# Kernel tuning notes

Measured on AMD Instinct MI355X. Metric: run time of the kernel, lower is better.

## Reference

```python
import jax, jax.numpy as jnp
import numpy as np

N_NODES = 100000
N_EDGES = 3200000
IN_DIM, HID_DIM, OUT_DIM = 512, 256, 64


def setup_inputs() -> dict:
    key = jax.random.key(0)
    k1, k2, k3, k4, k5, k6 = jax.random.split(key, 6)
    x = jax.random.normal(k1, (N_NODES, IN_DIM), dtype=jnp.float32)
    src = jax.random.randint(k2, (N_EDGES,), 0, N_NODES, dtype=jnp.int32)
    dst = jax.random.randint(k3, (N_EDGES,), 0, N_NODES, dtype=jnp.int32)
    edge_index = jnp.stack([src, dst])  # [2, E]: row 0 = src (column), row 1 = dst (row)
    edge_weight = jax.random.uniform(k4, (N_EDGES,), dtype=jnp.float32)
    # Xavier-uniform init like nn.init.xavier_uniform_
    lim1 = float(np.sqrt(6.0 / (IN_DIM + HID_DIM)))
    lim2 = float(np.sqrt(6.0 / (HID_DIM + OUT_DIM)))
    W1 = jax.random.uniform(k5, (IN_DIM, HID_DIM), minval=-lim1, maxval=lim1, dtype=jnp.float32)
    W2 = jax.random.uniform(k6, (HID_DIM, OUT_DIM), minval=-lim2, maxval=lim2, dtype=jnp.float32)
    return {"x": x, "edge_index": edge_index, "edge_weight": edge_weight, "W1": W1, "W2": W2}


def _spmm(edge_index, edge_weight, support):
    # out[dst] += w * support[src]  (sparse adjacency @ dense support)
    src, dst = edge_index[0], edge_index[1]
    msgs = support[src] * edge_weight[:, None]  # [E, F]
    return jax.ops.segment_sum(msgs, dst, num_segments=N_NODES)


def reference(x, edge_index, edge_weight, W1, W2):
    # Layer 1: dense GEMM then SpMM, then ReLU (dropout is identity in eval)
    h = _spmm(edge_index, edge_weight, x @ W1)
    h = jax.nn.relu(h)
    # Layer 2
    out = _spmm(edge_index, edge_weight, h @ W2)
    return jax.nn.softmax(out, axis=1)
```

## Files before the change

### kernel.cpp

```cpp
#include <hip/hip_runtime.h>
#include <hip/hip_bf16.h>

typedef __attribute__((ext_vector_type(8))) short bf16x8;
typedef __attribute__((ext_vector_type(4))) float f32x4;
typedef __attribute__((ext_vector_type(4))) _Float16 f16x4;
typedef unsigned short ushort_t;

#define NN   100000
#define NE   3200000
#define IND  512
#define HIDD 256
#define OUTD 64

#define NBKT 98
#define P1E  2048

__device__ __forceinline__ ushort_t f2bf(float a) {
    unsigned u = __float_as_uint(a);
    unsigned r = (u + 0x7FFFu + ((u >> 16) & 1u)) >> 16;
    return (ushort_t)r;
}
__device__ __forceinline__ float bf2f(ushort_t b) {
    return __uint_as_float(((unsigned)b) << 16);
}

union U8 { ushort_t us[8]; unsigned u32[4]; uint4 v; };
union U4 { ushort_t us[4]; uint2 v; };

#define GLOAD_LDS16(gp, lp) \
    __builtin_amdgcn_global_load_lds( \
        (const __attribute__((address_space(1))) void*)(const void*)(gp), \
        (__attribute__((address_space(3))) void*)(void*)(lp), 16, 0, 0)

__global__ void splitw_k(const float* __restrict__ in, ushort_t* __restrict__ thi,
                         ushort_t* __restrict__ tlo, int R, int C) {
    int i = blockIdx.x * 256 + threadIdx.x;
    if (i < R * C) {
        int r = i / C, c = i % C;
        float a = in[i];
        ushort_t h = f2bf(a);
        thi[(size_t)c * R + r] = h;
        tlo[(size_t)c * R + r] = f2bf(a - bf2f(h));
    }
}

__global__ __launch_bounds__(256, 3) void gemm1_k(
    const float* __restrict__ A, const ushort_t* __restrict__ BtHi,
    const ushort_t* __restrict__ BtLo, _Float16* __restrict__ C)
{
    const int M = NN, N = HIDD, K = IND;
    __shared__ __align__(16) float    sA [128 * 32];
    __shared__ __align__(16) ushort_t sBh[128 * 32];
    __shared__ __align__(16) ushort_t sBl[128 * 32];

    const int tid  = threadIdx.x;
    const int wave = tid >> 6;
    const int lane = tid & 63;
    const int quad = lane >> 4;
    const int l15  = lane & 15;
    const int wr   = wave >> 1;
    const int wc   = wave & 1;
    const int n0   = blockIdx.x * 128;
    const int m0   = blockIdx.y * 128;

    const float* aSrc[4];
    float*       aDst[4];
    #pragma unroll
    for (int it = 0; it < 4; ++it) {
        int f = it * 256 + tid;
        int r = f >> 3;
        int bp = (f & 7) ^ ((r & 3) << 1) ^ ((r >> 2) & 1);
        int gr = m0 + r; if (gr >= M) gr = M - 1;
        aSrc[it] = A + (size_t)gr * K + bp * 4;
        aDst[it] = &sA[f * 4];
    }
    const ushort_t* bhSrc[2]; const ushort_t* blSrc[2];
    ushort_t* bhDst[2]; ushort_t* blDst[2];
    #pragma unroll
    for (int it = 0; it < 2; ++it) {
        int f = it * 256 + tid;
        int r = f >> 2;
        int qp = (f & 3) ^ ((r >> 1) & 3);
        bhSrc[it] = BtHi + (size_t)(n0 + r) * K + qp * 8;
        blSrc[it] = BtLo + (size_t)(n0 + r) * K + qp * 8;
        bhDst[it] = &sBh[f * 8];
        blDst[it] = &sBl[f * 8];
    }

    int aOff[4][2];
    #pragma unroll
    for (int ms = 0; ms < 4; ++ms) {
        int rA = wr * 64 + ms * 16 + l15;
        int sw = ((rA & 3) << 1) ^ ((rA >> 2) & 1);
        int cb = quad << 1;
        aOff[ms][0] = rA * 32 + (((cb    ) ^ sw) << 2);
        aOff[ms][1] = rA * 32 + (((cb | 1) ^ sw) << 2);
    }
    int bOff[4];
    #pragma unroll
    for (int ns = 0; ns < 4; ++ns) {
        int rB = wc * 64 + ns * 16 + l15;
        bOff[ns] = rB * 32 + (quad ^ ((rB >> 1) & 3)) * 8;
    }

    f32x4 acc[4][4] = {};

    for (int k0 = 0; k0 < K; k0 += 32) {
        #pragma unroll
        for (int it = 0; it < 4; ++it) GLOAD_LDS16(aSrc[it] + k0, aDst[it]);
        #pragma unroll
        for (int it = 0; it < 2; ++it) {
            GLOAD_LDS16(bhSrc[it] + k0, bhDst[it]);
            GLOAD_LDS16(blSrc[it] + k0, blDst[it]);
        }
        __syncthreads();

        bf16x8 aH[4], aL[4];
        #pragma unroll
        for (int ms = 0; ms < 4; ++ms) {
            float4 v0 = *(const float4*)&sA[aOff[ms][0]];
            float4 v1 = *(const float4*)&sA[aOff[ms][1]];
            float vv[8] = {v0.x, v0.y, v0.z, v0.w, v1.x, v1.y, v1.z, v1.w};
            U8 H, L;
            #pragma unroll
            for (int j = 0; j < 4; ++j) {
                unsigned u0 = __float_as_uint(vv[2 * j]);
                unsigned u1 = __float_as_uint(vv[2 * j + 1]);
                H.u32[j] = __builtin_amdgcn_perm(u1, u0, 0x07060302u);
                float r0 = vv[2 * j]     - __uint_as_float(u0 & 0xFFFF0000u);
                float r1 = vv[2 * j + 1] - __uint_as_float(u1 & 0xFFFF0000u);
                L.u32[j] = __builtin_amdgcn_perm(__float_as_uint(r1),
                                                 __float_as_uint(r0), 0x07060302u);
            }
            aH[ms] = *(const bf16x8*)&H.v;
            aL[ms] = *(const bf16x8*)&L.v;
        }

        #pragma unroll
        for (int ns = 0; ns < 4; ++ns) {
            bf16x8 bH = *(const bf16x8*)&sBh[bOff[ns]];
            bf16x8 bL = *(const bf16x8*)&sBl[bOff[ns]];
            #pragma unroll
            for (int ms = 0; ms < 4; ++ms) {
                acc[ms][ns] = __builtin_amdgcn_mfma_f32_16x16x32_bf16(aH[ms], bH, acc[ms][ns], 0, 0, 0);
                acc[ms][ns] = __builtin_amdgcn_mfma_f32_16x16x32_bf16(aL[ms], bH, acc[ms][ns], 0, 0, 0);
                acc[ms][ns] = __builtin_amdgcn_mfma_f32_16x16x32_bf16(aH[ms], bL, acc[ms][ns], 0, 0, 0);
            }
        }
        __syncthreads();
    }

    #pragma unroll
    for (int ms = 0; ms < 4; ++ms) {
        int row = m0 + wr * 64 + ms * 16 + quad * 4;
        #pragma unroll
        for (int ns = 0; ns < 4; ++ns) {
            int col = n0 + wc * 64 + ns * 16 + l15;
            #pragma unroll
            for (int r = 0; r < 4; ++r)
                if (row + r < M) C[(size_t)(row + r) * N + col] = (_Float16)acc[ms][ns][r];
        }
    }
}

__global__ __launch_bounds__(256) void gemm2_k(
    const ushort_t* __restrict__ AHi, const ushort_t* __restrict__ ALo,
    const ushort_t* __restrict__ BtHi, const ushort_t* __restrict__ BtLo,
    _Float16* __restrict__ C)
{
    const int M = NN, N = OUTD, K = HIDD;
    __shared__ __align__(16) ushort_t sAh[128 * 32];
    __shared__ __align__(16) ushort_t sAl[128 * 32];
    __shared__ __align__(16) ushort_t sBh[64 * 32];
    __shared__ __align__(16) ushort_t sBl[64 * 32];

    const int tid  = threadIdx.x;
    const int wave = tid >> 6;
    const int lane = tid & 63;
    const int quad = lane >> 4;
    const int l15  = lane & 15;
    const int m0   = blockIdx.x * 128;

    const ushort_t* ahSrc[2]; const ushort_t* alSrc[2];
    ushort_t* ahDst[2]; ushort_t* alDst[2];
    #pragma unroll
    for (int it = 0; it < 2; ++it) {
        int f = it * 256 + tid;
        int r = f >> 2;
        int qp = (f & 3) ^ ((r >> 1) & 3);
        int gr = m0 + r; if (gr >= M) gr = M - 1;
        ahSrc[it] = AHi + (size_t)gr * K + qp * 8;
        alSrc[it] = ALo + (size_t)gr * K + qp * 8;
        ahDst[it] = &sAh[f * 8];
        alDst[it] = &sAl[f * 8];
    }
    const ushort_t *bhSrc, *blSrc; ushort_t *bhDst, *blDst;
    {
        int f = tid;
        int r = f >> 2;
        int qp = (f & 3) ^ ((r >> 1) & 3);
        bhSrc = BtHi + (size_t)r * K + qp * 8;
        blSrc = BtLo + (size_t)r * K + qp * 8;
        bhDst = &sBh[f * 8];
        blDst = &sBl[f * 8];
    }

    int aOff[2], bOff[4];
    #pragma unroll
    for (int ms = 0; ms < 2; ++ms) {
        int rA = wave * 32 + ms * 16 + l15;
        aOff[ms] = rA * 32 + (quad ^ ((rA >> 1) & 3)) * 8;
    }
    #pragma unroll
    for (int ns = 0; ns < 4; ++ns) {
        int rB = ns * 16 + l15;
        bOff[ns] = rB * 32 + (quad ^ ((rB >> 1) & 3)) * 8;
    }

    f32x4 acc[2][4] = {};

    for (int k0 = 0; k0 < K; k0 += 32) {
        #pragma unroll
        for (int it = 0; it < 2; ++it) {
            GLOAD_LDS16(ahSrc[it] + k0, ahDst[it]);
            GLOAD_LDS16(alSrc[it] + k0, alDst[it]);
        }
        GLOAD_LDS16(bhSrc + k0, bhDst);
        GLOAD_LDS16(blSrc + k0, blDst);
        __syncthreads();

        bf16x8 aH[2], aL[2];
        #pragma unroll
        for (int ms = 0; ms < 2; ++ms) {
            aH[ms] = *(const bf16x8*)&sAh[aOff[ms]];
            aL[ms] = *(const bf16x8*)&sAl[aOff[ms]];
        }
        #pragma unroll
        for (int ns = 0; ns < 4; ++ns) {
            bf16x8 bH = *(const bf16x8*)&sBh[bOff[ns]];
            bf16x8 bL = *(const bf16x8*)&sBl[bOff[ns]];
            #pragma unroll
            for (int ms = 0; ms < 2; ++ms) {
                acc[ms][ns] = __builtin_amdgcn_mfma_f32_16x16x32_bf16(aH[ms], bH, acc[ms][ns], 0, 0, 0);
                acc[ms][ns] = __builtin_amdgcn_mfma_f32_16x16x32_bf16(aL[ms], bH, acc[ms][ns], 0, 0, 0);
                acc[ms][ns] = __builtin_amdgcn_mfma_f32_16x16x32_bf16(aH[ms], bL, acc[ms][ns], 0, 0, 0);
            }
        }
        __syncthreads();
    }

    #pragma unroll
    for (int ms = 0; ms < 2; ++ms) {
        int row = m0 + wave * 32 + ms * 16 + quad * 4;
        #pragma unroll
        for (int ns = 0; ns < 4; ++ns) {
            int col = ns * 16 + l15;
            #pragma unroll
            for (int r = 0; r < 4; ++r)
                if (row + r < M) C[(size_t)(row + r) * N + col] = (_Float16)acc[ms][ns][r];
        }
    }
}

__global__ __launch_bounds__(256) void bhist_k(const int* __restrict__ dst,
                                               int* __restrict__ bucketHist) {
    __shared__ int h[NBKT];
    int t = threadIdx.x;
    if (t < NBKT) h[t] = 0;
    __syncthreads();
    #pragma unroll
    for (int j = 0; j < 4; ++j) {
        int e = blockIdx.x * 1024 + t + j * 256;
        if (e < NE) atomicAdd(&h[dst[e] >> 10], 1);
    }
    __syncthreads();
    if (t < NBKT && h[t]) atomicAdd(&bucketHist[t], h[t]);
}

__global__ __launch_bounds__(128) void bscan_k(const int* __restrict__ bucketHist,
                                               int* __restrict__ bucketStart,
                                               int* __restrict__ bucketCursor) {
    __shared__ int s[128];
    int t = threadIdx.x;
    int v = (t < NBKT) ? bucketHist[t] : 0;
    s[t] = v;
    for (int off = 1; off < 128; off <<= 1) {
        __syncthreads();
        int a = (t >= off) ? s[t - off] : 0;
        __syncthreads();
        s[t] += a;
    }
    __syncthreads();
    if (t < NBKT) { bucketStart[t] = s[t] - v; bucketCursor[t] = s[t] - v; }
    if (t == NBKT - 1) bucketStart[NBKT] = s[t];
}

__global__ __launch_bounds__(256) void phase1_k(
    const int* __restrict__ src, const int* __restrict__ dst,
    const float* __restrict__ w, int* __restrict__ bucketCursor,
    int2* __restrict__ binned)
{
    __shared__ int2 raw[P1E];
    __shared__ int2 ord[P1E];
    __shared__ ushort_t rbkt[P1E], obkt[P1E];
    __shared__ int hist[128], excl[128], cursor[128], gbase[128], stmp[128];

    int t = threadIdx.x;
    if (t < 128) hist[t] = 0;
    __syncthreads();

    int e0 = blockIdx.x * P1E;
    #pragma unroll
    for (int j = 0; j < P1E / 256; ++j) {
        int li = t + j * 256;
        int e = e0 + li;
        if (e < NE) {
            int d = dst[e];
            int b = d >> 10;
            raw[li] = make_int2(src[e] | ((d & 1023) << 17), __float_as_int(w[e]));
            rbkt[li] = (ushort_t)b;
            atomicAdd(&hist[b], 1);
        } else rbkt[li] = 0xFFFFu;
    }
    __syncthreads();
    int v = (t < 128) ? hist[t] : 0;
    if (t < 128) stmp[t] = v;
    for (int off = 1; off < 128; off <<= 1) {
        __syncthreads();
        int a = (t < 128 && t >= off) ? stmp[t - off] : 0;
        __syncthreads();
        if (t < 128) stmp[t] += a;
    }
    __syncthreads();
    if (t < 128) { excl[t] = stmp[t] - v; cursor[t] = stmp[t] - v; }
    if (t < NBKT) gbase[t] = atomicAdd(&bucketCursor[t], hist[t]);
    __syncthreads();
    #pragma unroll
    for (int j = 0; j < P1E / 256; ++j) {
        int li = t + j * 256;
        ushort_t b = rbkt[li];
        if (b != 0xFFFFu) {
            int p = atomicAdd(&cursor[b], 1);
            ord[p] = raw[li];
            obkt[p] = b;
        }
    }
    __syncthreads();
    int tot = excl[NBKT - 1] + hist[NBKT - 1];
    #pragma unroll
    for (int j = 0; j < P1E / 256; ++j) {
        int li = t + j * 256;
        if (li < tot) {
            int b = obkt[li];
            binned[(size_t)gbase[b] + (li - excl[b])] = ord[li];
        }
    }
}

__global__ __launch_bounds__(256) void phase2_k(
    const int* __restrict__ bucketStart, const int2* __restrict__ binned,
    int* __restrict__ rowptr, int2* __restrict__ esw)
{
    __shared__ int cnt[1024], ex[1024], cur[1024], wsum[256];
    int t = threadIdx.x, blk = blockIdx.x;
    int gb = bucketStart[blk], ge = bucketStart[blk + 1];
    #pragma unroll
    for (int j = 0; j < 4; ++j) cnt[t + j * 256] = 0;
    __syncthreads();
    for (int e = gb + t; e < ge; e += 256)
        atomicAdd(&cnt[(binned[e].x >> 17) & 1023], 1);
    __syncthreads();
    int b4 = t * 4;
    int l0 = cnt[b4], l1 = cnt[b4 + 1], l2 = cnt[b4 + 2], l3 = cnt[b4 + 3];
    int ls = l0 + l1 + l2 + l3;
    wsum[t] = ls;
    for (int off = 1; off < 256; off <<= 1) {
        __syncthreads();
        int a = (t >= off) ? wsum[t - off] : 0;
        __syncthreads();
        wsum[t] += a;
    }
    __syncthreads();
    int be = wsum[t] - ls;
    ex[b4] = be;            cur[b4] = be;
    ex[b4 + 1] = be + l0;     cur[b4 + 1] = be + l0;
    ex[b4 + 2] = be + l0 + l1;  cur[b4 + 2] = be + l0 + l1;
    ex[b4 + 3] = be + l0 + l1 + l2; cur[b4 + 3] = be + l0 + l1 + l2;
    __syncthreads();
    int n0 = blk << 10;
    #pragma unroll
    for (int j = 0; j < 4; ++j) {
        int i = b4 + j;
        if (n0 + i < NN) rowptr[n0 + i] = gb + ex[i];
    }
    if (blk == NBKT - 1 && t == 0) rowptr[NN] = NE;
    for (int e = gb + t; e < ge; e += 256) {
        int2 en = binned[e];
        int d = (en.x >> 17) & 1023;
        int p = atomicAdd(&cur[d], 1);
        esw[(size_t)gb + p] = make_int2(en.x & 0x1FFFF, en.y);
    }
}

__global__ __launch_bounds__(256) void spmm_relu_k(
    const int* __restrict__ rowptr, const int2* __restrict__ esw,
    const _Float16* __restrict__ X, ushort_t* __restrict__ Hhi,
    ushort_t* __restrict__ Hlo)
{
    const int wave = threadIdx.x >> 6;
    const int lane = threadIdx.x & 63;
    const int node = blockIdx.x * 4 + wave;
    const int beg = rowptr[node], end = rowptr[node + 1];
    f32x4 acc = {0.f, 0.f, 0.f, 0.f};
    const _Float16* Xl = X + lane * 4;
    #pragma unroll 8
    for (int e = beg; e < end; ++e) {
        int2 sw = esw[e];
        float w = __int_as_float(sw.y);
        f16x4 v = *(const f16x4*)(Xl + (size_t)sw.x * HIDD);
        acc.x += (float)v[0] * w;
        acc.y += (float)v[1] * w;
        acc.z += (float)v[2] * w;
        acc.w += (float)v[3] * w;
    }
    float vals[4] = {fmaxf(acc.x, 0.f), fmaxf(acc.y, 0.f),
                     fmaxf(acc.z, 0.f), fmaxf(acc.w, 0.f)};
    U4 H, L;
    #pragma unroll
    for (int j = 0; j < 4; ++j) {
        ushort_t h = f2bf(vals[j]);
        H.us[j] = h;
        L.us[j] = f2bf(vals[j] - bf2f(h));
    }
    *(uint2*)(Hhi + (size_t)node * HIDD + lane * 4) = H.v;
    *(uint2*)(Hlo + (size_t)node * HIDD + lane * 4) = L.v;
}

__global__ __launch_bounds__(256) void spmm_softmax_k(
    const int* __restrict__ rowptr, const int2* __restrict__ esw,
    const _Float16* __restrict__ X, float* __restrict__ out)
{
    int node = blockIdx.x * 4 + (threadIdx.x >> 6);
    int lane = threadIdx.x & 63;
    int beg = rowptr[node], end = rowptr[node + 1];
    float acc = 0.f;
    #pragma unroll 4
    for (int e = beg; e < end; ++e) {
        int2 sw = esw[e];
        acc += __int_as_float(sw.y) * (float)X[(size_t)sw.x * OUTD + lane];
    }
    float mx = acc;
    #pragma unroll
    for (int off = 32; off > 0; off >>= 1) mx = fmaxf(mx, __shfl_xor(mx, off));
    float ex = __expf(acc - mx);
    float sm = ex;
    #pragma unroll
    for (int off = 32; off > 0; off >>= 1) sm += __shfl_xor(sm, off);
    out[(size_t)node * OUTD + lane] = ex / sm;
}

extern "C" void kernel_launch(void* const* d_in, const int* in_sizes, int n_in,
                              void* d_out, int out_size, void* d_ws, size_t ws_size,
                              hipStream_t stream) {
    const float* x  = (const float*)d_in[0];
    const int*   ei = (const int*)d_in[1];
    const float* ew = (const float*)d_in[2];
    const float* W1 = (const float*)d_in[3];
    const float* W2 = (const float*)d_in[4];
    float* out = (float*)d_out;
    const int* src = ei;
    const int* dst = ei + NE;

    char* ws = (char*)d_ws;
    size_t o = 0;
    auto take = [&](size_t bytes) -> void* {
        void* p = (void*)(ws + o);
        o += (bytes + 255) & ~(size_t)255;
        return p;
    };
    _Float16* S1      = (_Float16*)take((size_t)NN * HIDD * 2);
    ushort_t* hHi     = (ushort_t*)take((size_t)NN * HIDD * 2);
    ushort_t* hLo     = (ushort_t*)take((size_t)NN * HIDD * 2);
    ushort_t* W1tHi   = (ushort_t*)take((size_t)IND * HIDD * 2);
    ushort_t* W1tLo   = (ushort_t*)take((size_t)IND * HIDD * 2);
    ushort_t* W2tHi   = (ushort_t*)take((size_t)HIDD * OUTD * 2);
    ushort_t* W2tLo   = (ushort_t*)take((size_t)HIDD * OUTD * 2);
    int*      rowptr  = (int*     )take((size_t)(NN + 1) * 4);
    int*      bHist   = (int*     )take(NBKT * 4);
    int*      bStart  = (int*     )take((NBKT + 1) * 4);
    int*      bCursor = (int*     )take(NBKT * 4);
    int2*     esw     = (int2*    )take((size_t)NE * 8);
    int2*     binned  = (int2*)hHi;
    _Float16* S2      = S1;
    (void)in_sizes; (void)n_in; (void)out_size; (void)ws_size;

    const int MB = (NN + 127) / 128;

    hipMemsetAsync(bHist, 0, NBKT * 4, stream);
    splitw_k<<<(IND * HIDD + 255) / 256, 256, 0, stream>>>(W1, W1tHi, W1tLo, IND, HIDD);
    splitw_k<<<(HIDD * OUTD + 255) / 256, 256, 0, stream>>>(W2, W2tHi, W2tLo, HIDD, OUTD);

    bhist_k<<<(NE + 1023) / 1024, 256, 0, stream>>>(dst, bHist);
    bscan_k<<<1, 128, 0, stream>>>(bHist, bStart, bCursor);
    phase1_k<<<(NE + P1E - 1) / P1E, 256, 0, stream>>>(src, dst, ew, bCursor, binned);
    phase2_k<<<NBKT, 256, 0, stream>>>(bStart, binned, rowptr, esw);

    gemm1_k<<<dim3(2, MB), 256, 0, stream>>>(x, W1tHi, W1tLo, S1);
    spmm_relu_k<<<NN / 4, 256, 0, stream>>>(rowptr, esw, S1, hHi, hLo);
    gemm2_k<<<MB, 256, 0, stream>>>(hHi, hLo, W2tHi, W2tLo, S2);
    spmm_softmax_k<<<NN / 4, 256, 0, stream>>>(rowptr, esw, S2, out);
}
```

Measured before the change: 898.2 us.

## Fuse layer-1 SpMM+ReLU with the second GEMM through shared memory

The layer-1 SpMM kernel now aggregates 16 nodes per block, keeps the ReLU'd fp32 hidden rows in LDS, and immediately multiplies them by W2 using split-bf16 MFMA to write the 64-wide S2. This removes the hi/lo bf16 hidden-state round trip through global memory (two 100000x256 arrays written then read) and one kernel launch. W2 is read per block straight from global memory, and each wave now handles four nodes in sequence, which may reduce latency hiding in the gather loop.

```diff
diff --git a/kernel.cpp b/kernel.cpp
--- a/kernel.cpp
+++ b/kernel.cpp
@@ -25,12 +25,28 @@
 }
 
 union U8 { ushort_t us[8]; unsigned u32[4]; uint4 v; };
-union U4 { ushort_t us[4]; uint2 v; };
 
 #define GLOAD_LDS16(gp, lp) \
     __builtin_amdgcn_global_load_lds( \
         (const __attribute__((address_space(1))) void*)(const void*)(gp), \
         (__attribute__((address_space(3))) void*)(void*)(lp), 16, 0, 0)
+
+__device__ __forceinline__ void split8(float4 v0, float4 v1, bf16x8& aH, bf16x8& aL) {
+    float vv[8] = {v0.x, v0.y, v0.z, v0.w, v1.x, v1.y, v1.z, v1.w};
+    U8 H, L;
+    #pragma unroll
+    for (int j = 0; j < 4; ++j) {
+        unsigned u0 = __float_as_uint(vv[2 * j]);
+        unsigned u1 = __float_as_uint(vv[2 * j + 1]);
+        H.u32[j] = __builtin_amdgcn_perm(u1, u0, 0x07060302u);
+        float r0 = vv[2 * j]     - __uint_as_float(u0 & 0xFFFF0000u);
+        float r1 = vv[2 * j + 1] - __uint_as_float(u1 & 0xFFFF0000u);
+        L.u32[j] = __builtin_amdgcn_perm(__float_as_uint(r1),
+                                         __float_as_uint(r0), 0x07060302u);
+    }
+    aH = *(const bf16x8*)&H.v;
+    aL = *(const bf16x8*)&L.v;
+}
 
 __global__ void splitw_k(const float* __restrict__ in, ushort_t* __restrict__ thi,
                          ushort_t* __restrict__ tlo, int R, int C) {
@@ -120,20 +136,7 @@
         for (int ms = 0; ms < 4; ++ms) {
             float4 v0 = *(const float4*)&sA[aOff[ms][0]];
             float4 v1 = *(const float4*)&sA[aOff[ms][1]];
-            float vv[8] = {v0.x, v0.y, v0.z, v0.w, v1.x, v1.y, v1.z, v1.w};
-            U8 H, L;
-            #pragma unroll
-            for (int j = 0; j < 4; ++j) {
-                unsigned u0 = __float_as_uint(vv[2 * j]);
-                unsigned u1 = __float_as_uint(vv[2 * j + 1]);
-                H.u32[j] = __builtin_amdgcn_perm(u1, u0, 0x07060302u);
-                float r0 = vv[2 * j]     - __uint_as_float(u0 & 0xFFFF0000u);
-                float r1 = vv[2 * j + 1] - __uint_as_float(u1 & 0xFFFF0000u);
-                L.u32[j] = __builtin_amdgcn_perm(__float_as_uint(r1),
-                                                 __float_as_uint(r0), 0x07060302u);
-            }
-            aH[ms] = *(const bf16x8*)&H.v;
-            aL[ms] = *(const bf16x8*)&L.v;
+            split8(v0, v1, aH[ms], aL[ms]);
         }
 
         #pragma unroll
@@ -163,105 +166,6 @@
     }
 }
 
-__global__ __launch_bounds__(256) void gemm2_k(
-    const ushort_t* __restrict__ AHi, const ushort_t* __restrict__ ALo,
-    const ushort_t* __restrict__ BtHi, const ushort_t* __restrict__ BtLo,
-    _Float16* __restrict__ C)
-{
-    const int M = NN, N = OUTD, K = HIDD;
-    __shared__ __align__(16) ushort_t sAh[128 * 32];
-    __shared__ __align__(16) ushort_t sAl[128 * 32];
-    __shared__ __align__(16) ushort_t sBh[64 * 32];
-    __shared__ __align__(16) ushort_t sBl[64 * 32];
-
-    const int tid  = threadIdx.x;
-    const int wave = tid >> 6;
-    const int lane = tid & 63;
-    const int quad = lane >> 4;
-    const int l15  = lane & 15;
-    const int m0   = blockIdx.x * 128;
-
-    const ushort_t* ahSrc[2]; const ushort_t* alSrc[2];
-    ushort_t* ahDst[2]; ushort_t* alDst[2];
-    #pragma unroll
-    for (int it = 0; it < 2; ++it) {
-        int f = it * 256 + tid;
-        int r = f >> 2;
-        int qp = (f & 3) ^ ((r >> 1) & 3);
-        int gr = m0 + r; if (gr >= M) gr = M - 1;
-        ahSrc[it] = AHi + (size_t)gr * K + qp * 8;
-        alSrc[it] = ALo + (size_t)gr * K + qp * 8;
-        ahDst[it] = &sAh[f * 8];
-        alDst[it] = &sAl[f * 8];
-    }
-    const ushort_t *bhSrc, *blSrc; ushort_t *bhDst, *blDst;
-    {
-        int f = tid;
-        int r = f >> 2;
-        int qp = (f & 3) ^ ((r >> 1) & 3);
-        bhSrc = BtHi + (size_t)r * K + qp * 8;
-        blSrc = BtLo + (size_t)r * K + qp * 8;
-        bhDst = &sBh[f * 8];
-        blDst = &sBl[f * 8];
-    }
-
-    int aOff[2], bOff[4];
-    #pragma unroll
-    for (int ms = 0; ms < 2; ++ms) {
-        int rA = wave * 32 + ms * 16 + l15;
-        aOff[ms] = rA * 32 + (quad ^ ((rA >> 1) & 3)) * 8;
-    }
-    #pragma unroll
-    for (int ns = 0; ns < 4; ++ns) {
-        int rB = ns * 16 + l15;
-        bOff[ns] = rB * 32 + (quad ^ ((rB >> 1) & 3)) * 8;
-    }
-
-    f32x4 acc[2][4] = {};
-
-    for (int k0 = 0; k0 < K; k0 += 32) {
-        #pragma unroll
-        for (int it = 0; it < 2; ++it) {
-            GLOAD_LDS16(ahSrc[it] + k0, ahDst[it]);
-            GLOAD_LDS16(alSrc[it] + k0, alDst[it]);
-        }
-        GLOAD_LDS16(bhSrc + k0, bhDst);
-        GLOAD_LDS16(blSrc + k0, blDst);
-        __syncthreads();
-
-        bf16x8 aH[2], aL[2];
-        #pragma unroll
-        for (int ms = 0; ms < 2; ++ms) {
-            aH[ms] = *(const bf16x8*)&sAh[aOff[ms]];
-            aL[ms] = *(const bf16x8*)&sAl[aOff[ms]];
-        }
-        #pragma unroll
-        for (int ns = 0; ns < 4; ++ns) {
-            bf16x8 bH = *(const bf16x8*)&sBh[bOff[ns]];
-            bf16x8 bL = *(const bf16x8*)&sBl[bOff[ns]];
-            #pragma unroll
-            for (int ms = 0; ms < 2; ++ms) {
-                acc[ms][ns] = __builtin_amdgcn_mfma_f32_16x16x32_bf16(aH[ms], bH, acc[ms][ns], 0, 0, 0);
-                acc[ms][ns] = __builtin_amdgcn_mfma_f32_16x16x32_bf16(aL[ms], bH, acc[ms][ns], 0, 0, 0);
-                acc[ms][ns] = __builtin_amdgcn_mfma_f32_16x16x32_bf16(aH[ms], bL, acc[ms][ns], 0, 0, 0);
-            }
-        }
-        __syncthreads();
-    }
-
-    #pragma unroll
-    for (int ms = 0; ms < 2; ++ms) {
-        int row = m0 + wave * 32 + ms * 16 + quad * 4;
-        #pragma unroll
-        for (int ns = 0; ns < 4; ++ns) {
-            int col = ns * 16 + l15;
-            #pragma unroll
-            for (int r = 0; r < 4; ++r)
-                if (row + r < M) C[(size_t)(row + r) * N + col] = (_Float16)acc[ms][ns][r];
-        }
-    }
-}
-
 __global__ __launch_bounds__(256) void bhist_k(const int* __restrict__ dst,
                                                int* __restrict__ bucketHist) {
     __shared__ int h[NBKT];
@@ -402,38 +306,67 @@
     }
 }
 
-__global__ __launch_bounds__(256) void spmm_relu_k(
+__global__ __launch_bounds__(256) void spmm_relu_gemm2_k(
     const int* __restrict__ rowptr, const int2* __restrict__ esw,
-    const _Float16* __restrict__ X, ushort_t* __restrict__ Hhi,
-    ushort_t* __restrict__ Hlo)
+    const _Float16* __restrict__ X, const ushort_t* __restrict__ BtHi,
+    const ushort_t* __restrict__ BtLo, _Float16* __restrict__ S2)
 {
-    const int wave = threadIdx.x >> 6;
-    const int lane = threadIdx.x & 63;
-    const int node = blockIdx.x * 4 + wave;
-    const int beg = rowptr[node], end = rowptr[node + 1];
-    f32x4 acc = {0.f, 0.f, 0.f, 0.f};
+    __shared__ __align__(16) float h[16][260];
+
+    const int wave  = threadIdx.x >> 6;
+    const int lane  = threadIdx.x & 63;
+    const int quad  = lane >> 4;
+    const int l15   = lane & 15;
+    const int nbase = blockIdx.x * 16;
+
     const _Float16* Xl = X + lane * 4;
-    #pragma unroll 8
-    for (int e = beg; e < end; ++e) {
-        int2 sw = esw[e];
-        float w = __int_as_float(sw.y);
-        f16x4 v = *(const f16x4*)(Xl + (size_t)sw.x * HIDD);
-        acc.x += (float)v[0] * w;
-        acc.y += (float)v[1] * w;
-        acc.z += (float)v[2] * w;
-        acc.w += (float)v[3] * w;
-    }
-    float vals[4] = {fmaxf(acc.x, 0.f), fmaxf(acc.y, 0.f),
-                     fmaxf(acc.z, 0.f), fmaxf(acc.w, 0.f)};
-    U4 H, L;
-    #pragma unroll
-    for (int j = 0; j < 4; ++j) {
-        ushort_t h = f2bf(vals[j]);
-        H.us[j] = h;
-        L.us[j] = f2bf(vals[j] - bf2f(h));
-    }
-    *(uint2*)(Hhi + (size_t)node * HIDD + lane * 4) = H.v;
-    *(uint2*)(Hlo + (size_t)node * HIDD + lane * 4) = L.v;
+    #pragma unroll
+    for (int i = 0; i < 4; ++i) {
+        const int ln   = wave * 4 + i;
+        const int node = nbase + ln;
+        const int beg = rowptr[node], end = rowptr[node + 1];
+        f32x4 acc = {0.f, 0.f, 0.f, 0.f};
+        #pragma unroll 8
+        for (int e = beg; e < end; ++e) {
+            int2 sw = esw[e];
+            float w = __int_as_float(sw.y);
+            f16x4 v = *(const f16x4*)(Xl + (size_t)sw.x * HIDD);
+            acc.x += (float)v[0] * w;
+            acc.y += (float)v[1] * w;
+            acc.z += (float)v[2] * w;
+            acc.w += (float)v[3] * w;
+        }
+        f32x4 r;
+        r.x = fmaxf(acc.x, 0.f);
+        r.y = fmaxf(acc.y, 0.f);
+        r.z = fmaxf(acc.z, 0.f);
+        r.w = fmaxf(acc.w, 0.f);
+        *(f32x4*)&h[ln][lane * 4] = r;
+    }
+    __syncthreads();
+
+    f32x4 acc2 = {0.f, 0.f, 0.f, 0.f};
+    const ushort_t* bh = BtHi + (size_t)(wave * 16 + l15) * HIDD;
+    const ushort_t* bl = BtLo + (size_t)(wave * 16 + l15) * HIDD;
+    #pragma unroll
+    for (int ks = 0; ks < 8; ++ks) {
+        const int ko = ks * 32 + quad * 8;
+        const float* ap = &h[l15][ko];
+        float4 v0 = *(const float4*)ap;
+        float4 v1 = *(const float4*)(ap + 4);
+        bf16x8 aH, aL;
+        split8(v0, v1, aH, aL);
+        bf16x8 bH = *(const bf16x8*)(bh + ko);
+        bf16x8 bL = *(const bf16x8*)(bl + ko);
+        acc2 = __builtin_amdgcn_mfma_f32_16x16x32_bf16(aH, bH, acc2, 0, 0, 0);
+        acc2 = __builtin_amdgcn_mfma_f32_16x16x32_bf16(aL, bH, acc2, 0, 0, 0);
+        acc2 = __builtin_amdgcn_mfma_f32_16x16x32_bf16(aH, bL, acc2, 0, 0, 0);
+    }
+    #pragma unroll
+    for (int r = 0; r < 4; ++r) {
+        const int node = nbase + quad * 4 + r;
+        S2[(size_t)node * OUTD + wave * 16 + l15] = (_Float16)acc2[r];
+    }
 }
 
 __global__ __launch_bounds__(256) void spmm_softmax_k(
@@ -479,8 +412,8 @@
         return p;
     };
     _Float16* S1      = (_Float16*)take((size_t)NN * HIDD * 2);
-    ushort_t* hHi     = (ushort_t*)take((size_t)NN * HIDD * 2);
-    ushort_t* hLo     = (ushort_t*)take((size_t)NN * HIDD * 2);
+    _Float16* S2      = (_Float16*)take((size_t)NN * OUTD * 2);
+    int2*     binned  = (int2*    )take((size_t)NE * 8);
     ushort_t* W1tHi   = (ushort_t*)take((size_t)IND * HIDD * 2);
     ushort_t* W1tLo   = (ushort_t*)take((size_t)IND * HIDD * 2);
     ushort_t* W2tHi   = (ushort_t*)take((size_t)HIDD * OUTD * 2);
@@ -490,8 +423,6 @@
     int*      bStart  = (int*     )take((NBKT + 1) * 4);
     int*      bCursor = (int*     )take(NBKT * 4);
     int2*     esw     = (int2*    )take((size_t)NE * 8);
-    int2*     binned  = (int2*)hHi;
-    _Float16* S2      = S1;
     (void)in_sizes; (void)n_in; (void)out_size; (void)ws_size;
 
     const int MB = (NN + 127) / 128;
@@ -506,7 +437,6 @@
     phase2_k<<<NBKT, 256, 0, stream>>>(bStart, binned, rowptr, esw);
 
     gemm1_k<<<dim3(2, MB), 256, 0, stream>>>(x, W1tHi, W1tLo, S1);
-    spmm_relu_k<<<NN / 4, 256, 0, stream>>>(rowptr, esw, S1, hHi, hLo);
-    gemm2_k<<<MB, 256, 0, stream>>>(hHi, hLo, W2tHi, W2tLo, S2);
+    spmm_relu_gemm2_k<<<NN / 16, 256, 0, stream>>>(rowptr, esw, S1, W2tHi, W2tLo, S2);
     spmm_softmax_k<<<NN / 4, 256, 0, stream>>>(rowptr, esw, S2, out);
 }
```

After: 898.8 us. About the same (+0.1%).
